# Kernel tuning notes

Hardware: AMD Instinct MI355X
Metric: run time of the kernel (lower is better)

The kernel has to match this reference:

```python
import jax, jax.numpy as jnp
import numpy as np

E, C, N, W_IN, W_OUT = 5, 2, 2048, 512, 256


def setup_inputs() -> dict:
    key = jax.random.key(0)
    ks = jax.random.split(key, 11)
    A = jax.random.uniform(ks[0], (E, N, N), dtype=jnp.float32)  # stacked edge-type adjacencies
    X = jax.random.normal(ks[1], (N, W_IN), dtype=jnp.float32)
    # GTConv weights (out_channels=C, in_channels=E), init std=0.01 as in torch
    gt_w0a = 0.01 * jax.random.normal(ks[2], (C, E), dtype=jnp.float32)
    gt_w0b = 0.01 * jax.random.normal(ks[3], (C, E), dtype=jnp.float32)
    gt_w1 = 0.01 * jax.random.normal(ks[4], (C, E), dtype=jnp.float32)
    gcn_w = jax.random.normal(ks[5], (W_IN, W_OUT), dtype=jnp.float32) / np.sqrt(W_IN)
    gcn_b = jnp.zeros((W_OUT,), dtype=jnp.float32)
    lin1_w = 0.02 * jax.random.normal(ks[6], (W_OUT, C * W_OUT), dtype=jnp.float32)
    lin1_b = jnp.zeros((W_OUT,), dtype=jnp.float32)
    lin2_w = 0.02 * jax.random.normal(ks[7], (W_OUT, W_OUT), dtype=jnp.float32)
    lin2_b = jnp.zeros((W_OUT,), dtype=jnp.float32)
    return {"A": A, "X": X, "gt_w0a": gt_w0a, "gt_w0b": gt_w0b, "gt_w1": gt_w1,
            "gcn_w": gcn_w, "gcn_b": gcn_b, "lin1_w": lin1_w, "lin1_b": lin1_b,
            "lin2_w": lin2_w, "lin2_b": lin2_b}


def _gtconv(w, A):
    # softmax over edge types, weighted sum of adjacencies == coalesce of scaled edge lists
    f = jax.nn.softmax(w, axis=1)  # (C, E)
    return jnp.einsum('ce,enm->cnm', f, A)  # (C, N, N)


def _normalize(H):
    # remove self loops, then divide each entry by its column (target) degree
    n = H.shape[-1]
    H = H * (1.0 - jnp.eye(n, dtype=H.dtype))
    deg = H.sum(axis=-2)                      # (C, N) column sums == scatter_add over col
    safe = jnp.where(deg != 0, deg, 1.0)
    dinv = jnp.where(deg != 0, 1.0 / safe, 0.0)
    return H * dinv[:, None, :]


def reference(A, X, gt_w0a, gt_w0b, gt_w1, gcn_w, gcn_b, lin1_w, lin1_b, lin2_w, lin2_b):
    # layer 0 (first=True): two GTConvs, per-channel spspmm == batched matmul
    Ha = _gtconv(gt_w0a, A)
    Hb = _gtconv(gt_w0b, A)
    H = _normalize(jnp.einsum('cij,cjk->cik', Ha, Hb))
    # layer 1 (first=False): H_ @ conv1(A)
    Hb2 = _gtconv(gt_w1, A)
    H = _normalize(jnp.einsum('cij,cjk->cik', H, Hb2))
    # GCNConv per channel: add self loops, symmetric deg^{-1/2} normalization, aggregate to col
    n = H.shape[-1]
    M = H + jnp.eye(n, dtype=H.dtype)         # (C, N, N)
    deg = M.sum(axis=-2)                      # (C, N)
    safe = jnp.where(deg > 0, deg, 1.0)
    dis = jnp.where(deg > 0, safe ** -0.5, 0.0)
    Ahat = dis[:, :, None] * M * dis[:, None, :]
    XW = X @ gcn_w                            # (N, W_OUT)
    out = jnp.einsum('crn,rf->cnf', Ahat, XW) + gcn_b  # out[c,n] = sum_r Ahat[c,r,n] XW[r]
    out = jax.nn.relu(out)                    # (C, N, W_OUT)
    Xcat = out.transpose(1, 0, 2).reshape(n, -1)       # concat channels along dim=1
    h = jax.nn.relu(Xcat @ lin1_w.T + lin1_b)
    return h @ lin2_w.T + lin2_b
```

## Files before the change

### kernel.cpp

```cpp
#include <hip/hip_runtime.h>
#include <cstdint>
#include <cstddef>

#define NN   2048
#define N2   (2048LL*2048LL)
#define CC   2
#define EE   5
#define WIN  512
#define WOUT 256

typedef __bf16 bf16_t;
typedef __attribute__((ext_vector_type(8))) __bf16 bf16x8;
typedef __attribute__((ext_vector_type(4))) __bf16 bf16x4;
typedef __attribute__((ext_vector_type(4))) float  f32x4;

#define AS1 __attribute__((address_space(1)))
#define AS3 __attribute__((address_space(3)))


__global__ void k_combine(const float* __restrict__ A,
                          const float* __restrict__ w0a, const float* __restrict__ w0b,
                          const float* __restrict__ w1,
                          bf16_t* __restrict__ Ha, bf16_t* __restrict__ HbT,
                          bf16_t* __restrict__ Hb2T, float* __restrict__ part,
                          const float* __restrict__ X, const float* __restrict__ l1w,
                          const float* __restrict__ l2w, const float* __restrict__ gcnw,
                          bf16_t* __restrict__ Xb, bf16_t* __restrict__ l1wb,
                          bf16_t* __restrict__ l2wb, bf16_t* __restrict__ gwT) {
  __shared__ bf16_t tl[2][64][65];
  __shared__ float cs[2][4][64];
  int bid = blockIdx.x;
  int t = threadIdx.x;

  if (bid >= 1024) {
    int bid2 = bid - 1024;
    if (bid2 < 608) {
      int i = bid2 * 256 + t;
      const float* src; bf16_t* dst; int off;
      if (i < 131072)      { src = X;   dst = Xb;   off = i; }
      else if (i < 147456) { src = l1w; dst = l1wb; off = i - 131072; }
      else                 { src = l2w; dst = l2wb; off = i - 147456; }
      float4 a = ((const float4*)src)[off * 2];
      float4 b = ((const float4*)src)[off * 2 + 1];
      bf16x8 o;
      o[0] = (bf16_t)a.x; o[1] = (bf16_t)a.y; o[2] = (bf16_t)a.z; o[3] = (bf16_t)a.w;
      o[4] = (bf16_t)b.x; o[5] = (bf16_t)b.y; o[6] = (bf16_t)b.z; o[7] = (bf16_t)b.w;
      ((bf16x8*)dst)[off] = o;
    } else {
      int b2 = bid2 - 608;
      int m0 = (b2 & 7) * 64, n0 = (b2 >> 3) * 64;
      int tr = t >> 4, tc = (t & 15) << 2;
      bf16_t (*tile)[65] = (bf16_t (*)[65])&tl[0][0][0];
#pragma unroll
      for (int v = 0; v < 4; ++v) {
        int r = tr + v * 16;
        float4 d = *(const float4*)&gcnw[(long long)(m0 + r) * WOUT + n0 + tc];
        tile[r][tc + 0] = (bf16_t)d.x; tile[r][tc + 1] = (bf16_t)d.y;
        tile[r][tc + 2] = (bf16_t)d.z; tile[r][tc + 3] = (bf16_t)d.w;
      }
      __syncthreads();
#pragma unroll
      for (int v = 0; v < 4; ++v) {
        int r = tr + v * 16;
        bf16x4 o;
        o[0] = tile[tc + 0][r]; o[1] = tile[tc + 1][r];
        o[2] = tile[tc + 2][r]; o[3] = tile[tc + 3][r];
        *(bf16x4*)&gwT[(long long)(n0 + r) * WIN + m0 + tc] = o;
      }
    }
    return;
  }

  float f[3][2][5];
  {
    const float* wp[3] = {w0a, w0b, w1};
#pragma unroll
    for (int w = 0; w < 3; ++w)
#pragma unroll
      for (int c = 0; c < 2; ++c) {
        float x[5], m = -1e30f, s = 0.f;
#pragma unroll
        for (int e = 0; e < 5; ++e) { x[e] = wp[w][c * 5 + e]; m = fmaxf(m, x[e]); }
#pragma unroll
        for (int e = 0; e < 5; ++e) { x[e] = expf(x[e] - m); s += x[e]; }
#pragma unroll
        for (int e = 0; e < 5; ++e) f[w][c][e] = x[e] / s;
      }
  }
  int i0 = (bid >> 5) * 64, j0 = (bid & 31) * 64;
  int tr = t >> 4, tc = (t & 15) << 2;
  int lane = t & 63, wid = t >> 6;
  float cs0[4] = {0, 0, 0, 0}, cs1[4] = {0, 0, 0, 0};
  bf16x4 hb2a[4], hb2b[4];

#pragma unroll
  for (int v = 0; v < 4; ++v) {
    int lr = tr + v * 16;
    long long gi = i0 + lr;
    const float* base = A + gi * (long long)NN + j0 + tc;
    float av[5][4];
#pragma unroll
    for (int e = 0; e < 5; ++e) {
      float4 q = *(const float4*)(base + (long long)e * N2);
      av[e][0] = q.x; av[e][1] = q.y; av[e][2] = q.z; av[e][3] = q.w;
    }
    bf16x4 ha0, ha1;
#pragma unroll
    for (int x = 0; x < 4; ++x) {
      float s0 = 0.f, s1 = 0.f, s2 = 0.f, s3 = 0.f, s4 = 0.f, s5 = 0.f;
#pragma unroll
      for (int e = 0; e < 5; ++e) {
        float u = av[e][x];
        s0 += f[0][0][e] * u; s1 += f[0][1][e] * u;
        s2 += f[1][0][e] * u; s3 += f[1][1][e] * u;
        s4 += f[2][0][e] * u; s5 += f[2][1][e] * u;
      }
      ha0[x] = (bf16_t)s0; cs0[x] += (float)ha0[x];
      ha1[x] = (bf16_t)s1; cs1[x] += (float)ha1[x];
      tl[0][lr][tc + x] = (bf16_t)s2; tl[1][lr][tc + x] = (bf16_t)s3;
      hb2a[v][x] = (bf16_t)s4; hb2b[v][x] = (bf16_t)s5;
    }
    *(bf16x4*)&Ha[0 * N2 + gi * NN + j0 + tc] = ha0;
    *(bf16x4*)&Ha[1 * N2 + gi * NN + j0 + tc] = ha1;
  }
#pragma unroll
  for (int x = 0; x < 4; ++x) {
    float a0 = cs0[x], a1 = cs1[x];
    a0 += __shfl_xor(a0, 16, 64); a0 += __shfl_xor(a0, 32, 64);
    a1 += __shfl_xor(a1, 16, 64); a1 += __shfl_xor(a1, 32, 64);
    if ((lane >> 4) == 0) {
      cs[0][wid][(lane & 15) * 4 + x] = a0;
      cs[1][wid][(lane & 15) * 4 + x] = a1;
    }
  }
  __syncthreads();

#pragma unroll
  for (int v = 0; v < 4; ++v) {
    int lr = tr + v * 16;
#pragma unroll
    for (int ch = 0; ch < 2; ++ch) {
      bf16x4 o;
      o[0] = tl[ch][tc + 0][lr]; o[1] = tl[ch][tc + 1][lr];
      o[2] = tl[ch][tc + 2][lr]; o[3] = tl[ch][tc + 3][lr];
      *(bf16x4*)&HbT[(long long)ch * N2 + (long long)(j0 + lr) * NN + i0 + tc] = o;
    }
  }
  if (t < 128) {
    int ch = t >> 6, col = t & 63;
    float s = cs[ch][0][col] + cs[ch][1][col] + cs[ch][2][col] + cs[ch][3][col];
    part[((long long)ch * 32 + (bid >> 5)) * NN + j0 + col] = s;
  }
  __syncthreads();

#pragma unroll
  for (int v = 0; v < 4; ++v) {
    int lr = tr + v * 16;
#pragma unroll
    for (int x = 0; x < 4; ++x) {
      tl[0][lr][tc + x] = hb2a[v][x];
      tl[1][lr][tc + x] = hb2b[v][x];
    }
  }
  __syncthreads();

#pragma unroll
  for (int v = 0; v < 4; ++v) {
    int lr = tr + v * 16;
#pragma unroll
    for (int ch = 0; ch < 2; ++ch) {
      bf16x4 o;
      o[0] = tl[ch][tc + 0][lr]; o[1] = tl[ch][tc + 1][lr];
      o[2] = tl[ch][tc + 2][lr]; o[3] = tl[ch][tc + 3][lr];
      *(bf16x4*)&Hb2T[(long long)ch * N2 + (long long)(j0 + lr) * NN + i0 + tc] = o;
    }
  }
}

__global__ void k_s_finish(const float* __restrict__ part, float* __restrict__ s) {
  int idx = blockIdx.x * 256 + threadIdx.x;
  int c = idx >> 11, k = idx & 2047;
  float acc = 0.f;
#pragma unroll
  for (int ib = 0; ib < 32; ++ib) acc += part[((long long)c * 32 + ib) * NN + k];
  s[idx] = acc;
}

template<bool EMIT_DIS>
__global__ void k_deg(const float* __restrict__ svec, const bf16_t* __restrict__ Arows,
                      const bf16_t* __restrict__ BT,
                      float* __restrict__ out1, float* __restrict__ out2,
                      float* __restrict__ out3) {
  int c = blockIdx.y;
  int j = blockIdx.x * 4 + (threadIdx.x >> 6);
  int lane = threadIdx.x & 63;
  const bf16_t* a = Arows + (long long)c * N2 + (long long)j * NN;
  const bf16_t* b = BT + (long long)c * N2 + (long long)j * NN;
  const float* s = svec + c * NN;
  float acc_s = 0.f, acc_a = 0.f;
#pragma unroll
  for (int it = 0; it < 4; ++it) {
    int k0 = (lane + it * 64) * 8;
    bf16x8 av = *(const bf16x8*)(a + k0);
    bf16x8 bv = *(const bf16x8*)(b + k0);
    float4 s0 = *(const float4*)(s + k0);
    float4 s1 = *(const float4*)(s + k0 + 4);
    float sv[8] = {s0.x, s0.y, s0.z, s0.w, s1.x, s1.y, s1.z, s1.w};
#pragma unroll
    for (int x = 0; x < 8; ++x) {
      float bx = (float)bv[x];
      acc_s += sv[x] * bx;
      acc_a += (float)av[x] * bx;
    }
  }
#pragma unroll
  for (int o = 32; o > 0; o >>= 1) {
    acc_s += __shfl_xor(acc_s, o, 64);
    acc_a += __shfl_xor(acc_a, o, 64);
  }
  if (lane == 0) {
    float deg = acc_s - acc_a;
    bool nz = (deg != 0.f);
    if (!EMIT_DIS) {
      out1[c * NN + j] = nz ? 1.f / deg : 0.f;
      out2[c * NN + j] = nz ? 1.f : 0.f;
    } else {
      float dis = nz ? 0.70710678118654752f : 1.f;
      out1[c * NN + j] = nz ? dis / deg : 0.f;
      out2[c * NN + j] = dis;
      out3[c * NN + j] = acc_a;
    }
  }
}


__global__ __launch_bounds__(256)
void k_gemmL(const bf16_t* __restrict__ A, const bf16_t* __restrict__ B,
             bf16_t* __restrict__ Hn, bf16_t* __restrict__ HnT,
             const float* __restrict__ dinv) {
  __shared__ __align__(16) char smem[65536];
  bf16_t* As = (bf16_t*)smem;
  bf16_t* Bs = (bf16_t*)(smem + 32768);
  bf16_t* tile = (bf16_t*)smem;

  int cz = blockIdx.z;
  const bf16_t* Ab = A + cz * N2 + (long long)blockIdx.x * 128 * NN;
  const bf16_t* Bb = B + cz * N2 + (long long)blockIdx.y * 128 * NN;

  int t = threadIdx.x, wid = t >> 6, lane = t & 63;
  int wr = wid >> 1, wc = wid & 1;
  f32x4 acc[4][4] = {};
  int frow = lane & 15;
  int fk_sw = (((lane >> 4) ^ ((frow >> 1) & 3)) << 3);
  int srow = t >> 2;
  int scol_sw = (((t & 3) ^ ((t >> 3) & 3)) << 3);

  auto STAGE = [&](int TT, int BUF) {
#pragma unroll
    for (int s = 0; s < 2; ++s) {
      long long kko = (long long)TT * 64 + s * 32 + scol_sw;
      const bf16_t* ga0 = Ab + (long long)srow * NN + kko;
      const bf16_t* gb0 = Bb + (long long)srow * NN + kko;
      char* la = smem + BUF * 16384 + s * 8192 + wid * 1024;
      char* lb = smem + 32768 + BUF * 16384 + s * 8192 + wid * 1024;
      __builtin_amdgcn_global_load_lds((AS1 void*)ga0, (AS3 void*)la, 16, 0, 0);
      __builtin_amdgcn_global_load_lds((AS1 void*)(ga0 + 64LL * NN), (AS3 void*)(la + 4096), 16, 0, 0);
      __builtin_amdgcn_global_load_lds((AS1 void*)gb0, (AS3 void*)lb, 16, 0, 0);
      __builtin_amdgcn_global_load_lds((AS1 void*)(gb0 + 64LL * NN), (AS3 void*)(lb + 4096), 16, 0, 0);
    }
  };
  auto COMPUTE = [&](int BUF) {
#pragma unroll
    for (int ks = 0; ks < 2; ++ks) {
      bf16x8 af[4], bfr[4];
#pragma unroll
      for (int m = 0; m < 4; ++m)
        af[m] = *(const bf16x8*)&As[BUF * 8192 + ks * 4096 + (wr * 64 + m * 16 + frow) * 32 + fk_sw];
#pragma unroll
      for (int n = 0; n < 4; ++n)
        bfr[n] = *(const bf16x8*)&Bs[BUF * 8192 + ks * 4096 + (wc * 64 + n * 16 + frow) * 32 + fk_sw];
      __builtin_amdgcn_s_setprio(1);
#pragma unroll
      for (int m = 0; m < 4; ++m)
#pragma unroll
        for (int n = 0; n < 4; ++n)
          acc[m][n] = __builtin_amdgcn_mfma_f32_16x16x32_bf16(af[m], bfr[n], acc[m][n], 0, 0, 0);
      __builtin_amdgcn_s_setprio(0);
    }
  };

  const int nt = 32;
  STAGE(0, 0); STAGE(1, 1);
  for (int tt = 0; tt < nt; ++tt) {
    if (tt < nt - 1) asm volatile("s_waitcnt vmcnt(8)" ::: "memory");
    else             asm volatile("s_waitcnt vmcnt(0)" ::: "memory");
    __builtin_amdgcn_s_barrier();
    __builtin_amdgcn_sched_barrier(0);
    COMPUTE(tt & 1);
    __builtin_amdgcn_s_barrier();
    if (tt + 2 < nt) STAGE(tt + 2, tt & 1);
  }
  __builtin_amdgcn_sched_barrier(0);

  int rl0 = wr * 64 + ((lane >> 4) << 2);
  int cl0 = wc * 64 + (lane & 15);
  int r0 = blockIdx.x * 128 + rl0;
  int c0 = blockIdx.y * 128 + cl0;

  bf16_t* Cb = Hn + cz * N2;
  bf16_t* Ct = HnT + cz * N2;
  float dj[4];
#pragma unroll
  for (int n = 0; n < 4; ++n) dj[n] = dinv[cz * NN + c0 + n * 16];
#pragma unroll
  for (int m = 0; m < 4; ++m)
#pragma unroll
    for (int n = 0; n < 4; ++n)
#pragma unroll
      for (int j = 0; j < 4; ++j) {
        int r = r0 + m * 16 + j, col = c0 + n * 16;
        float v = (r == col) ? 0.f : acc[m][n][j] * dj[n];
        Cb[(long long)r * NN + col] = (bf16_t)v;
        tile[(rl0 + m * 16 + j) * 130 + cl0 + n * 16] = (bf16_t)v;
      }
  __syncthreads();
  int nl = t >> 5, rl = (t & 31) * 4;
#pragma unroll
  for (int vv = 0; vv < 16; ++vv) {
    int n_l = nl + vv * 8;
    bf16x4 o;
    o[0] = tile[(rl + 0) * 130 + n_l]; o[1] = tile[(rl + 1) * 130 + n_l];
    o[2] = tile[(rl + 2) * 130 + n_l]; o[3] = tile[(rl + 3) * 130 + n_l];
    *(bf16x4*)&Ct[(long long)(blockIdx.y * 128 + n_l) * NN + blockIdx.x * 128 + rl] = o;
  }
}


enum { EP_BRELU = 3, EP_BF32 = 4, EP_BF16O = 7, EP_XWDT = 8, EP_GCN = 9 };

template<int EP>
__global__ __launch_bounds__(256)
void k_gemm(const bf16_t* __restrict__ A, const bf16_t* __restrict__ B,
            void* __restrict__ Cv,
            const float* __restrict__ aux1, const float* __restrict__ aux2,
            bf16_t* __restrict__ aux3, const float* __restrict__ aux4,
            int N, int K, int lda, int ldb,
            long long zA, long long zB, long long zC) {
  __shared__ __align__(16) char smem[36864];
  bf16_t* As = (bf16_t*)smem;
  bf16_t* Bs = (bf16_t*)(smem + 24576);
  bf16_t* tile = (bf16_t*)smem;

  int cz = blockIdx.z;
  const bf16_t* Ab = A + cz * zA + (long long)blockIdx.x * 128 * lda;
  const bf16_t* Bb = B + cz * zB + (long long)blockIdx.y * 64 * ldb;

  int t = threadIdx.x, wid = t >> 6, lane = t & 63;
  int wr = wid >> 1, wc = wid & 1;
  f32x4 acc[4][2] = {};
  int frow = lane & 15;
  int fk_sw = (((lane >> 4) ^ ((frow >> 1) & 3)) << 3);
  int srow = t >> 2;
  int scol_sw = (((t & 3) ^ ((t >> 3) & 3)) << 3);
  int nt = K >> 5;

  auto STAGE = [&](int TT, int BUF) {
    long long kko = (long long)TT * 32 + scol_sw;
    const bf16_t* ga0 = Ab + (long long)srow * lda + kko;
    const bf16_t* ga1 = Ab + (long long)(64 + srow) * lda + kko;
    const bf16_t* gb0 = Bb + (long long)srow * ldb + kko;
    char* la = smem + BUF * 8192 + wid * 1024;
    char* lb = smem + 24576 + BUF * 4096 + wid * 1024;
    __builtin_amdgcn_global_load_lds((AS1 void*)ga0, (AS3 void*)la, 16, 0, 0);
    __builtin_amdgcn_global_load_lds((AS1 void*)ga1, (AS3 void*)(la + 4096), 16, 0, 0);
    __builtin_amdgcn_global_load_lds((AS1 void*)gb0, (AS3 void*)lb, 16, 0, 0);
  };
  auto COMPUTE = [&](int BUF) {
    bf16x8 af[4], bfr[2];
#pragma unroll
    for (int m = 0; m < 4; ++m)
      af[m] = *(const bf16x8*)&As[BUF * 4096 + (wr * 64 + m * 16 + frow) * 32 + fk_sw];
#pragma unroll
    for (int n = 0; n < 2; ++n)
      bfr[n] = *(const bf16x8*)&Bs[BUF * 2048 + (wc * 32 + n * 16 + frow) * 32 + fk_sw];
#pragma unroll
    for (int m = 0; m < 4; ++m)
#pragma unroll
      for (int n = 0; n < 2; ++n)
        acc[m][n] = __builtin_amdgcn_mfma_f32_16x16x32_bf16(af[m], bfr[n], acc[m][n], 0, 0, 0);
  };

  STAGE(0, 0); STAGE(1, 1); STAGE(2, 2);
  int slot = 0;
  for (int tt = 0; tt < nt; ++tt) {
    int rem = nt - 1 - tt;
    if (rem >= 2)      asm volatile("s_waitcnt vmcnt(6)" ::: "memory");
    else if (rem == 1) asm volatile("s_waitcnt vmcnt(3)" ::: "memory");
    else               asm volatile("s_waitcnt vmcnt(0)" ::: "memory");
    __builtin_amdgcn_s_barrier();
    __builtin_amdgcn_sched_barrier(0);
    COMPUTE(slot);
    __builtin_amdgcn_s_barrier();
    if (tt + 3 < nt) STAGE(tt + 3, slot);
    slot = (slot == 2) ? 0 : slot + 1;
  }
  __builtin_amdgcn_sched_barrier(0);

  int rl0 = wr * 64 + ((lane >> 4) << 2);
  int cl0 = wc * 32 + (lane & 15);
  int r0 = blockIdx.x * 128 + rl0;
  int c0 = blockIdx.y * 64 + cl0;

  if constexpr (EP == EP_BF16O) {
    bf16_t* Cb = (bf16_t*)Cv + cz * zC;
#pragma unroll
    for (int m = 0; m < 4; ++m)
#pragma unroll
      for (int n = 0; n < 2; ++n)
#pragma unroll
        for (int j = 0; j < 4; ++j)
          Cb[(long long)(r0 + m * 16 + j) * N + c0 + n * 16] = (bf16_t)acc[m][n][j];
  } else if constexpr (EP == EP_XWDT) {
    float* Cb = (float*)Cv;
#pragma unroll
    for (int m = 0; m < 4; ++m)
#pragma unroll
      for (int n = 0; n < 2; ++n)
#pragma unroll
        for (int j = 0; j < 4; ++j) {
          float v = acc[m][n][j];
          Cb[(long long)(r0 + m * 16 + j) * N + c0 + n * 16] = v;
          tile[(rl0 + m * 16 + j) * 65 + cl0 + n * 16] = (bf16_t)v;
        }
    __syncthreads();
    int nl = t >> 5, rl = (t & 31) * 4;
#pragma unroll
    for (int vv = 0; vv < 8; ++vv) {
      int n_l = nl + vv * 8;
      bf16x4 v4;
      v4[0] = tile[(rl + 0) * 65 + n_l]; v4[1] = tile[(rl + 1) * 65 + n_l];
      v4[2] = tile[(rl + 2) * 65 + n_l]; v4[3] = tile[(rl + 3) * 65 + n_l];
      int i0 = blockIdx.x * 128 + rl;
      long long row = (long long)(blockIdx.y * 64 + n_l) * NN + i0;
#pragma unroll
      for (int c = 0; c < 2; ++c) {
        float4 dv = *(const float4*)&aux2[c * NN + i0];
        bf16x4 o;
        o[0] = (bf16_t)((float)v4[0] * dv.x); o[1] = (bf16_t)((float)v4[1] * dv.y);
        o[2] = (bf16_t)((float)v4[2] * dv.z); o[3] = (bf16_t)((float)v4[3] * dv.w);
        *(bf16x4*)&aux3[(long long)c * WOUT * NN + row] = o;
      }
    }
  } else if constexpr (EP == EP_GCN) {
    bf16_t* Cb = (bf16_t*)Cv;
    const float* XWp = aux1;
    const float* csp = aux2 + cz * NN;
    const float* dnp = aux2 + CC * NN + cz * NN;
    const float* mdp = aux2 + 2 * CC * NN + cz * NN;
    float bj[2];
#pragma unroll
    for (int n = 0; n < 2; ++n) bj[n] = aux4[c0 + n * 16];
#pragma unroll
    for (int m = 0; m < 4; ++m)
#pragma unroll
      for (int j = 0; j < 4; ++j) {
        int r = r0 + m * 16 + j;
        float csv = csp[r], dnv = dnp[r], mdv = mdp[r];
        float mdd = mdv * dnv, d2 = dnv * dnv;
#pragma unroll
        for (int n = 0; n < 2; ++n) {
          float xw = XWp[(long long)r * WOUT + c0 + n * 16];
          float v = fmaxf(csv * (acc[m][n][j] - mdd * xw) + d2 * xw + bj[n], 0.f);
          Cb[(long long)r * (CC * WOUT) + cz * WOUT + c0 + n * 16] = (bf16_t)v;
        }
      }
  } else if constexpr (EP == EP_BRELU) {
    bf16_t* Cb = (bf16_t*)Cv;
    float bj[2];
#pragma unroll
    for (int n = 0; n < 2; ++n) bj[n] = aux1[c0 + n * 16];
#pragma unroll
    for (int m = 0; m < 4; ++m)
#pragma unroll
      for (int n = 0; n < 2; ++n)
#pragma unroll
        for (int j = 0; j < 4; ++j)
          Cb[(long long)(r0 + m * 16 + j) * N + c0 + n * 16] =
              (bf16_t)fmaxf(acc[m][n][j] + bj[n], 0.f);
  } else {
    float* Cb = (float*)Cv;
    float bj[2];
#pragma unroll
    for (int n = 0; n < 2; ++n) bj[n] = aux1[c0 + n * 16];
#pragma unroll
    for (int m = 0; m < 4; ++m)
#pragma unroll
      for (int n = 0; n < 2; ++n)
#pragma unroll
        for (int j = 0; j < 4; ++j)
          Cb[(long long)(r0 + m * 16 + j) * N + c0 + n * 16] = acc[m][n][j] + bj[n];
  }
}


extern "C" void kernel_launch(void* const* d_in, const int* in_sizes, int n_in,
                              void* d_out, int out_size, void* d_ws, size_t ws_size,
                              hipStream_t stream) {
  const float* A    = (const float*)d_in[0];
  const float* X    = (const float*)d_in[1];
  const float* w0a  = (const float*)d_in[2];
  const float* w0b  = (const float*)d_in[3];
  const float* w1   = (const float*)d_in[4];
  const float* gcnw = (const float*)d_in[5];
  const float* gcnb = (const float*)d_in[6];
  const float* l1w  = (const float*)d_in[7];
  const float* l1b  = (const float*)d_in[8];
  const float* l2w  = (const float*)d_in[9];
  const float* l2b  = (const float*)d_in[10];
  float* out = (float*)d_out;

  char* p = (char*)d_ws;
  auto carve = [&](size_t bytes) -> char* {
    char* r = p; p += (bytes + 255) & ~(size_t)255; return r;
  };
  float*  svec  = (float*)carve((size_t)CC * NN * 4);
  float*  dinv1 = (float*)carve((size_t)CC * NN * 4);
  float*  m1    = (float*)carve((size_t)CC * NN * 4);
  float*  scal  = (float*)carve((size_t)3 * CC * NN * 4);
  float*  part  = (float*)carve((size_t)CC * 32 * NN * 4);
  bf16_t* S1    = (bf16_t*)carve((size_t)CC * N2 * 2);
  bf16_t* HbT   = (bf16_t*)carve((size_t)CC * N2 * 2);
  bf16_t* Hb2T  = (bf16_t*)carve((size_t)CC * N2 * 2);
  bf16_t* Hn    = (bf16_t*)carve((size_t)CC * N2 * 2);
  bf16_t* HnT   = (bf16_t*)carve((size_t)CC * N2 * 2);
  bf16_t* Xb    = (bf16_t*)carve((size_t)NN * WIN * 2);
  bf16_t* gwT   = (bf16_t*)carve((size_t)WOUT * WIN * 2);
  bf16_t* l1wb  = (bf16_t*)carve((size_t)WOUT * CC * WOUT * 2);
  bf16_t* l2wb  = (bf16_t*)carve((size_t)WOUT * WOUT * 2);
  float*  XW    = (float*)carve((size_t)NN * WOUT * 4);
  bf16_t* Xcat  = (bf16_t*)carve((size_t)NN * CC * WOUT * 2);
  bf16_t* hb    = (bf16_t*)carve((size_t)NN * WOUT * 2);

  bf16_t* Ha = S1;
  bf16_t* XWdT = (bf16_t*)((char*)S1);
  bf16_t* Yt   = (bf16_t*)((char*)S1 + (2LL << 20));
  float*  disv = scal + CC * NN;

  k_combine<<<1664, 256, 0, stream>>>(A, w0a, w0b, w1, Ha, HbT, Hb2T, part,
                                      X, l1w, l2w, gcnw, Xb, l1wb, l2wb, gwT);
  k_s_finish<<<16, 256, 0, stream>>>(part, svec);

  k_deg<false><<<dim3(512, 2), 256, 0, stream>>>(svec, Ha, HbT, dinv1, m1, nullptr);
  k_gemmL<<<dim3(16, 16, 2), 256, 0, stream>>>(Ha, HbT, Hn, HnT, dinv1);

  k_deg<true><<<dim3(512, 2), 256, 0, stream>>>(m1, Hn, Hb2T,
                                                scal, scal + CC * NN, scal + 2 * CC * NN);

  k_gemm<EP_XWDT><<<dim3(16, 4, 1), 256, 0, stream>>>(
      Xb, gwT, XW, nullptr, disv, XWdT, nullptr, WOUT, WIN, WIN, WIN, 0, 0, 0);
  k_gemm<EP_BF16O><<<dim3(2, 32, 2), 256, 0, stream>>>(
      XWdT, HnT, Yt, nullptr, nullptr, nullptr, nullptr, NN, NN, NN, NN,
      (long long)WOUT * NN, N2, (long long)WOUT * NN);
  k_gemm<EP_GCN><<<dim3(16, 4, 2), 256, 0, stream>>>(
      Hb2T, Yt, Xcat, XW, scal, nullptr, gcnb, WOUT, NN, NN, NN,
      N2, (long long)WOUT * NN, 0);

  k_gemm<EP_BRELU><<<dim3(16, 4, 1), 256, 0, stream>>>(
      Xcat, l1wb, hb, l1b, nullptr, nullptr, nullptr, WOUT, CC * WOUT, CC * WOUT, CC * WOUT, 0, 0, 0);
  k_gemm<EP_BF32><<<dim3(16, 4, 1), 256, 0, stream>>>(
      hb, l2wb, out, l2b, nullptr, nullptr, nullptr, WOUT, WOUT, WOUT, WOUT, 0, 0, 0);
}
```

Measured before the change: 144.1 us.

## Give each wave private LDS staging to drop block barriers in GEMM loop

The GEMM main loop now has each wave load its own 64-row A and B slices into a private LDS region, with a K-step of 32 over 64 iterations. This removes the two block-wide barriers per iteration. The next stage's async loads are issued after the fragment reads complete, and a __syncthreads is added before the epilogue reuses LDS. The cost is that the two waves sharing a row or column block now each load the same data, doubling global-to-LDS traffic, and each iteration does half as much MFMA work.

```diff
diff --git a/kernel.cpp b/kernel.cpp
--- a/kernel.cpp
+++ b/kernel.cpp
@@ -239,66 +239,61 @@
              bf16_t* __restrict__ Hn, bf16_t* __restrict__ HnT,
              const float* __restrict__ dinv) {
   __shared__ __align__(16) char smem[65536];
-  bf16_t* As = (bf16_t*)smem;
-  bf16_t* Bs = (bf16_t*)(smem + 32768);
   bf16_t* tile = (bf16_t*)smem;
 
   int cz = blockIdx.z;
-  const bf16_t* Ab = A + cz * N2 + (long long)blockIdx.x * 128 * NN;
-  const bf16_t* Bb = B + cz * N2 + (long long)blockIdx.y * 128 * NN;
+  const bf16_t* Abase = A + cz * N2 + (long long)blockIdx.x * 128 * NN;
+  const bf16_t* Bbase = B + cz * N2 + (long long)blockIdx.y * 128 * NN;
 
   int t = threadIdx.x, wid = t >> 6, lane = t & 63;
   int wr = wid >> 1, wc = wid & 1;
   f32x4 acc[4][4] = {};
   int frow = lane & 15;
   int fk_sw = (((lane >> 4) ^ ((frow >> 1) & 3)) << 3);
-  int srow = t >> 2;
-  int scol_sw = (((t & 3) ^ ((t >> 3) & 3)) << 3);
+  int srw = lane >> 2;
+  int chunk_sw = ((lane & 3) ^ ((lane >> 3) & 3));
+  const bf16_t* Aw = Abase + (long long)(wr * 64 + srw) * NN + chunk_sw * 8;
+  const bf16_t* Bw = Bbase + (long long)(wc * 64 + srw) * NN + chunk_sw * 8;
+  char* lds0 = smem + wid * 16384;
 
   auto STAGE = [&](int TT, int BUF) {
-#pragma unroll
-    for (int s = 0; s < 2; ++s) {
-      long long kko = (long long)TT * 64 + s * 32 + scol_sw;
-      const bf16_t* ga0 = Ab + (long long)srow * NN + kko;
-      const bf16_t* gb0 = Bb + (long long)srow * NN + kko;
-      char* la = smem + BUF * 16384 + s * 8192 + wid * 1024;
-      char* lb = smem + 32768 + BUF * 16384 + s * 8192 + wid * 1024;
-      __builtin_amdgcn_global_load_lds((AS1 void*)ga0, (AS3 void*)la, 16, 0, 0);
-      __builtin_amdgcn_global_load_lds((AS1 void*)(ga0 + 64LL * NN), (AS3 void*)(la + 4096), 16, 0, 0);
-      __builtin_amdgcn_global_load_lds((AS1 void*)gb0, (AS3 void*)lb, 16, 0, 0);
-      __builtin_amdgcn_global_load_lds((AS1 void*)(gb0 + 64LL * NN), (AS3 void*)(lb + 4096), 16, 0, 0);
+    long long kk = (long long)TT * 32;
+    char* la = lds0 + BUF * 8192;
+    char* lb = la + 4096;
+#pragma unroll
+    for (int gl = 0; gl < 4; ++gl) {
+      __builtin_amdgcn_global_load_lds((AS1 void*)(Aw + (long long)(gl * 16) * NN + kk),
+          (AS3 void*)(la + gl * 1024), 16, 0, 0);
+      __builtin_amdgcn_global_load_lds((AS1 void*)(Bw + (long long)(gl * 16) * NN + kk),
+          (AS3 void*)(lb + gl * 1024), 16, 0, 0);
     }
   };
-  auto COMPUTE = [&](int BUF) {
-#pragma unroll
-    for (int ks = 0; ks < 2; ++ks) {
-      bf16x8 af[4], bfr[4];
-#pragma unroll
-      for (int m = 0; m < 4; ++m)
-        af[m] = *(const bf16x8*)&As[BUF * 8192 + ks * 4096 + (wr * 64 + m * 16 + frow) * 32 + fk_sw];
-#pragma unroll
-      for (int n = 0; n < 4; ++n)
-        bfr[n] = *(const bf16x8*)&Bs[BUF * 8192 + ks * 4096 + (wc * 64 + n * 16 + frow) * 32 + fk_sw];
-      __builtin_amdgcn_s_setprio(1);
-#pragma unroll
-      for (int m = 0; m < 4; ++m)
-#pragma unroll
-        for (int n = 0; n < 4; ++n)
-          acc[m][n] = __builtin_amdgcn_mfma_f32_16x16x32_bf16(af[m], bfr[n], acc[m][n], 0, 0, 0);
-      __builtin_amdgcn_s_setprio(0);
-    }
-  };
-
-  const int nt = 32;
+
+  const int nt = 64;
   STAGE(0, 0); STAGE(1, 1);
   for (int tt = 0; tt < nt; ++tt) {
     if (tt < nt - 1) asm volatile("s_waitcnt vmcnt(8)" ::: "memory");
     else             asm volatile("s_waitcnt vmcnt(0)" ::: "memory");
-    __builtin_amdgcn_s_barrier();
     __builtin_amdgcn_sched_barrier(0);
-    COMPUTE(tt & 1);
-    __builtin_amdgcn_s_barrier();
+    const bf16_t* As = (const bf16_t*)(lds0 + (tt & 1) * 8192);
+    const bf16_t* Bs = As + 2048;
+    bf16x8 af[4], bfr[4];
+#pragma unroll
+    for (int m = 0; m < 4; ++m)
+      af[m] = *(const bf16x8*)&As[(m * 16 + frow) * 32 + fk_sw];
+#pragma unroll
+    for (int n = 0; n < 4; ++n)
+      bfr[n] = *(const bf16x8*)&Bs[(n * 16 + frow) * 32 + fk_sw];
+    asm volatile("s_waitcnt lgkmcnt(0)" ::: "memory");
+    __builtin_amdgcn_sched_barrier(0);
     if (tt + 2 < nt) STAGE(tt + 2, tt & 1);
+    __builtin_amdgcn_s_setprio(1);
+#pragma unroll
+    for (int m = 0; m < 4; ++m)
+#pragma unroll
+      for (int n = 0; n < 4; ++n)
+        acc[m][n] = __builtin_amdgcn_mfma_f32_16x16x32_bf16(af[m], bfr[n], acc[m][n], 0, 0, 0);
+    __builtin_amdgcn_s_setprio(0);
   }
   __builtin_amdgcn_sched_barrier(0);
 
@@ -312,6 +307,7 @@
   float dj[4];
 #pragma unroll
   for (int n = 0; n < 4; ++n) dj[n] = dinv[cz * NN + c0 + n * 16];
+  __syncthreads();
 #pragma unroll
   for (int m = 0; m < 4; ++m)
 #pragma unroll
```

Result: slower. 164.9 us (+14.4%).
